# Kernel tuning notes

Hardware: AMD Instinct MI355X
Metric: run time of the kernel (lower is better)

The kernel has to match this reference:

```python
import jax, jax.numpy as jnp
import numpy as np

N_NODES = 20000
N_EDGES = 160000
IN_DIM = 2048
HID = 512


def setup_inputs() -> dict:
    key = jax.random.key(0)
    ks = jax.random.split(key, 12)
    s1 = 1.0 / np.sqrt(IN_DIM)
    s2 = 1.0 / np.sqrt(HID)
    return {
        "x": jax.random.normal(ks[0], (N_NODES, IN_DIM), dtype=jnp.float32),
        "edge_index": jax.random.randint(ks[1], (2, N_EDGES), 0, N_NODES, dtype=jnp.int64),
        "W1": jax.random.uniform(ks[2], (IN_DIM, HID), jnp.float32, -s1, s1),
        "b1": jax.random.uniform(ks[3], (HID,), jnp.float32, -s1, s1),
        "W2": jax.random.uniform(ks[4], (HID, HID), jnp.float32, -s2, s2),
        "b2": jax.random.uniform(ks[5], (HID,), jnp.float32, -s2, s2),
        "Wg": jax.random.uniform(ks[6], (HID, HID), jnp.float32, -s2, s2),
        "bg": jax.random.uniform(ks[7], (HID,), jnp.float32, -s2, s2),
        "Wa": jax.random.uniform(ks[8], (HID, 1), jnp.float32, -s2, s2),
        "ba": jax.random.uniform(ks[9], (1,), jnp.float32, -s2, s2),
    }


def reference(x, edge_index, W1, b1, W2, b2, Wg, bg, Wa, ba):
    # GINConv (eps=0): h = MLP((1+eps)*x + sum_{j in N(i)} x_j)
    src, dst = edge_index[0], edge_index[1]
    agg = jax.ops.segment_sum(x[src], dst, num_segments=x.shape[0])  # [N, IN_DIM]
    h = x + agg
    h = jnp.maximum(h @ W1 + b1, 0.0) @ W2 + b2  # [N, HID]
    # Gated attention pooling scores
    A = jnp.tanh(h @ Wg + bg)                    # [N, HID]
    alpha = (A @ Wa + ba)[:, 0]                  # [N]
    att_scores = jax.nn.softmax(alpha, axis=0)   # softmax over all nodes
    return (h, att_scores)
```

## Files before the change

### kernel.cpp

```cpp
#include <hip/hip_runtime.h>

typedef __attribute__((ext_vector_type(8))) __bf16 bf16x8;
typedef __attribute__((ext_vector_type(4))) float f32x4;
typedef __attribute__((ext_vector_type(8))) unsigned short u16x8;

__device__ __forceinline__ unsigned short f2b(float f) {
    union { float f; unsigned u; } v; v.f = f;
    unsigned r = v.u + 0x7FFFu + ((v.u >> 16) & 1u);
    return (unsigned short)(r >> 16);
}

__device__ __forceinline__ unsigned swz(int row, int s) {
    return (unsigned)((row * 64 + s * 16) ^ ((row & 8) << 2));
}

#define GLDS(g, l) __builtin_amdgcn_global_load_lds(                        \
    (const __attribute__((address_space(1))) void*)(g),                     \
    (__attribute__((address_space(3))) void*)(l), 16, 0, 0)

__global__ __launch_bounds__(256) void convw_pre_kernel(const float* __restrict__ W,
                                                        char* __restrict__ out, int K) {
    int t = blockIdx.x * 256 + threadIdx.x;
    if (t >= K * 512) return;
    int k = t >> 9, n = t & 511;
    int cb = n >> 8, r = n & 255, tt = k >> 5, s = (k & 31) >> 3, e = k & 7;
    size_t off = ((size_t)cb * (K >> 5) + tt) * 16384 + swz(r, s) + e * 2;
    *(unsigned short*)(out + off) = f2b(W[t]);
}

__global__ __launch_bounds__(256) void count_kernel(const int* __restrict__ dst,
                                                    int* __restrict__ counts, int E) {
    int e = blockIdx.x * 256 + threadIdx.x;
    if (e < E) atomicAdd(&counts[dst[e]], 1);
}

__global__ __launch_bounds__(1024) void scan_kernel(const int* __restrict__ counts,
                                                    int* __restrict__ offs, int N) {
    __shared__ int wsum[16], wpre[16];
    const int CH = 20;
    int tid = threadIdx.x, lane = tid & 63, wv = tid >> 6;
    int base = tid * CH;
    int s = 0;
    for (int i = 0; i < CH; i++) { int idx = base + i; s += (idx < N) ? counts[idx] : 0; }
    int run = s;
#pragma unroll
    for (int o = 1; o < 64; o <<= 1) { int v = __shfl_up(run, o, 64); if (lane >= o) run += v; }
    if (lane == 63) wsum[wv] = run;
    __syncthreads();
    if (tid == 0) { int acc = 0; for (int w = 0; w < 16; w++) { wpre[w] = acc; acc += wsum[w]; } }
    __syncthreads();
    int pre = wpre[wv] + (run - s);
    for (int i = 0; i < CH; i++) {
        int idx = base + i;
        if (idx <= N) offs[idx] = pre;
        pre += (idx < N) ? counts[idx] : 0;
    }
}

__global__ __launch_bounds__(256) void bucket_kernel(const int* __restrict__ src,
                                                     const int* __restrict__ dst,
                                                     const int* __restrict__ offs,
                                                     int* __restrict__ cursor,
                                                     int* __restrict__ eids, int E) {
    int e = blockIdx.x * 256 + threadIdx.x;
    if (e >= E) return;
    int d = dst[e];
    int pos = atomicAdd(&cursor[d], 1);
    eids[offs[d] + pos] = src[e];
}

__global__ __launch_bounds__(256) void gather_h1_kernel(const float* __restrict__ y,
                                                        const int* __restrict__ offs,
                                                        const int* __restrict__ eids,
                                                        const float* __restrict__ b1,
                                                        unsigned short* __restrict__ h1b,
                                                        int N) {
    int node = blockIdx.x * 2 + (threadIdx.x >> 7);
    if (node >= N) return;
    int c = (threadIdx.x & 127) << 2;
    float4 s = *(const float4*)(y + (size_t)node * 512 + c);
    int beg = offs[node], end = offs[node + 1];
    for (int k = beg; k < end; k++) {
        int sn = eids[k];
        const float4 v = *(const float4*)(y + (size_t)sn * 512 + c);
        s.x += v.x; s.y += v.y; s.z += v.z; s.w += v.w;
    }
    const float4 b = *(const float4*)(b1 + c);
    ushort4 o;
    o.x = f2b(fmaxf(s.x + b.x, 0.f));
    o.y = f2b(fmaxf(s.y + b.y, 0.f));
    o.z = f2b(fmaxf(s.z + b.z, 0.f));
    o.w = f2b(fmaxf(s.w + b.w, 0.f));
    ((ushort4*)h1b)[((size_t)node * 512 + c) >> 2] = o;
}

template <int KDIM, int AMODE, int EPI>
__global__ __launch_bounds__(256) void gemm_sec(const void* __restrict__ Asrc,
                                                const char* __restrict__ Bpre,
                                                const float* __restrict__ bias,
                                                float* __restrict__ Cf,
                                                char* __restrict__ hbpre,
                                                const float* __restrict__ Wa,
                                                float* __restrict__ alphaOut,
                                                int M) {
    constexpr int NT = KDIM / 32;
    __shared__ char smem[40960];
    const int tid = threadIdx.x, lane = tid & 63, wv = tid >> 6;
    const int fr = lane & 15, sec = lane >> 4, hi4 = (lane >> 4) * 4;
    const long row0 = (long)blockIdx.x * 64;
    const int cb = blockIdx.y;
    const char* Bp = Bpre + (size_t)cb * NT * 16384;

    f32x4 acc[4][4];
#pragma unroll
    for (int m = 0; m < 4; m++)
#pragma unroll
        for (int n = 0; n < 4; n++)
#pragma unroll
            for (int r = 0; r < 4; r++) acc[m][n][r] = 0.f;

    const int as_ = tid & 3, ar_ = tid >> 2;
    const unsigned awz = swz(ar_, as_);
    long arow = row0 + ar_; if (arow > (long)M - 1) arow = M - 1;
    const float* ApF = (const float*)Asrc + arow * KDIM + as_ * 8;
    const char*  ApH = (const char*)Asrc + arow * (KDIM * 2) + as_ * 16;
    const char*  ApT = (const char*)Asrc + (size_t)blockIdx.x * 65536;

#define ASEC(b) (smem + (b) * 4096)
#define BSEC(b) (smem + 8192 + (b) * 16384)
#define STAGE_B(buf, t) do {                                              \
        const char* src_ = Bp + (size_t)(t) * 16384;                      \
        _Pragma("unroll") for (int c_ = 0; c_ < 4; c_++)                  \
            GLDS(src_ + tid * 16 + c_ * 4096, BSEC(buf) + tid * 16 + c_ * 4096); \
    } while (0)

    STAGE_B(0, 0);
    if constexpr (AMODE == 0) {
        float4 a0 = *(const float4*)(ApF), a1 = *(const float4*)(ApF + 4);
        u16x8 o; o[0]=f2b(a0.x); o[1]=f2b(a0.y); o[2]=f2b(a0.z); o[3]=f2b(a0.w);
        o[4]=f2b(a1.x); o[5]=f2b(a1.y); o[6]=f2b(a1.z); o[7]=f2b(a1.w);
        *(u16x8*)(ASEC(0) + awz) = o;
    } else if constexpr (AMODE == 1) {
        u16x8 v = *(const u16x8*)(ApH);
        *(u16x8*)(ASEC(0) + awz) = v;
    } else {
        GLDS(ApT + tid * 16, ASEC(0) + tid * 16);
    }
    __syncthreads();

    for (int t = 0; t < NT; t++) {
        const int cur = t & 1, nxt = cur ^ 1;
        const bool more = (t + 1 < NT);
        float4 a0, a1; u16x8 av;
        if (more) {
            STAGE_B(nxt, t + 1);
            if constexpr (AMODE == 0) {
                a0 = *(const float4*)(ApF + (t + 1) * 32);
                a1 = *(const float4*)(ApF + (t + 1) * 32 + 4);
            } else if constexpr (AMODE == 1) {
                av = *(const u16x8*)(ApH + (t + 1) * 64);
            } else {
                GLDS(ApT + (size_t)(t + 1) * 4096 + tid * 16, ASEC(nxt) + tid * 16);
            }
        }
        bf16x8 wf[4], xf[4];
#pragma unroll
        for (int m = 0; m < 4; m++)
            wf[m] = *(const bf16x8*)(BSEC(cur) + swz(wv * 64 + m * 16 + fr, sec));
#pragma unroll
        for (int n = 0; n < 4; n++)
            xf[n] = *(const bf16x8*)(ASEC(cur) + swz(n * 16 + fr, sec));
#pragma unroll
        for (int m = 0; m < 4; m++)
#pragma unroll
            for (int n = 0; n < 4; n++)
                acc[m][n] = __builtin_amdgcn_mfma_f32_16x16x32_bf16(wf[m], xf[n], acc[m][n], 0, 0, 0);
        if (more) {
            if constexpr (AMODE == 0) {
                u16x8 o; o[0]=f2b(a0.x); o[1]=f2b(a0.y); o[2]=f2b(a0.z); o[3]=f2b(a0.w);
                o[4]=f2b(a1.x); o[5]=f2b(a1.y); o[6]=f2b(a1.z); o[7]=f2b(a1.w);
                *(u16x8*)(ASEC(nxt) + awz) = o;
            } else if constexpr (AMODE == 1) {
                *(u16x8*)(ASEC(nxt) + awz) = av;
            }
        }
        __syncthreads();
    }

    if constexpr (EPI == 0) {
#pragma unroll
        for (int n = 0; n < 4; n++) {
            long node = row0 + n * 16 + fr;
            if (node < M) {
#pragma unroll
                for (int m = 0; m < 4; m++)
                    *(f32x4*)(Cf + node * 512 + cb * 256 + wv * 64 + m * 16 + hi4) = acc[m][n];
            }
        }
    } else if constexpr (EPI == 1) {
#pragma unroll
        for (int n = 0; n < 4; n++) {
            int nodeloc = n * 16 + fr;
            long node = row0 + nodeloc;
#pragma unroll
            for (int m = 0; m < 4; m++) {
                int hc = cb * 256 + wv * 64 + m * 16 + hi4;
                f32x4 bv = *(const f32x4*)(bias + hc);
                f32x4 v = acc[m][n] + bv;
                if (node < M) *(f32x4*)(Cf + node * 512 + hc) = v;
                ushort4 o; o.x = f2b(v[0]); o.y = f2b(v[1]); o.z = f2b(v[2]); o.w = f2b(v[3]);
                int tt = hc >> 5, ss = (hc & 31) >> 3, e = hc & 7;
                *(ushort4*)(hbpre + (size_t)blockIdx.x * 65536 + (size_t)tt * 4096 +
                            swz(nodeloc, ss) + e * 2) = o;
            }
        }
    } else {
        float* aS = (float*)smem;
        if (tid < 64) aS[tid] = 0.f;
        __syncthreads();
#pragma unroll
        for (int n = 0; n < 4; n++) {
            float s = 0.f;
#pragma unroll
            for (int m = 0; m < 4; m++) {
                int gc = cb * 256 + wv * 64 + m * 16 + hi4;
                f32x4 bgv = *(const f32x4*)(bias + gc);
                f32x4 wav = *(const f32x4*)(Wa + gc);
#pragma unroll
                for (int r = 0; r < 4; r++)
                    s += tanhf(acc[m][n][r] + bgv[r]) * wav[r];
            }
            atomicAdd(&aS[n * 16 + fr], s);
        }
        __syncthreads();
        if (tid < 64) {
            long node = row0 + tid;
            if (node < M) atomicAdd(&alphaOut[node], aS[tid]);
        }
    }
#undef ASEC
#undef BSEC
#undef STAGE_B
}

__global__ __launch_bounds__(1024) void softmax_kernel(const float* __restrict__ alpha,
                                                       float* __restrict__ att, int N) {
    __shared__ float red[16];
    __shared__ float bc[2];
    int tid = threadIdx.x, lane = tid & 63, wv = tid >> 6;
    float m = -3.4e38f;
    for (int i = tid; i < N; i += 1024) m = fmaxf(m, alpha[i]);
#pragma unroll
    for (int o = 32; o > 0; o >>= 1) m = fmaxf(m, __shfl_xor(m, o, 64));
    if (lane == 0) red[wv] = m;
    __syncthreads();
    if (tid == 0) {
        float mm = red[0];
        for (int i = 1; i < 16; i++) mm = fmaxf(mm, red[i]);
        bc[0] = mm;
    }
    __syncthreads();
    float Mx = bc[0];
    float s = 0.f;
    for (int i = tid; i < N; i += 1024) s += expf(alpha[i] - Mx);
#pragma unroll
    for (int o = 32; o > 0; o >>= 1) s += __shfl_xor(s, o, 64);
    if (lane == 0) red[wv] = s;
    __syncthreads();
    if (tid == 0) {
        float ss = 0.f;
        for (int i = 0; i < 16; i++) ss += red[i];
        bc[1] = ss;
    }
    __syncthreads();
    float inv = 1.f / bc[1];
    for (int i = tid; i < N; i += 1024) att[i] = expf(alpha[i] - Mx) * inv;
}

extern "C" void kernel_launch(void* const* d_in, const int* in_sizes, int n_in,
                              void* d_out, int out_size, void* d_ws, size_t ws_size,
                              hipStream_t stream) {
    const float* x  = (const float*)d_in[0];
    const int*   ei = (const int*)d_in[1];
    const float* W1 = (const float*)d_in[2];
    const float* b1 = (const float*)d_in[3];
    const float* W2 = (const float*)d_in[4];
    const float* b2 = (const float*)d_in[5];
    const float* Wg = (const float*)d_in[6];
    const float* bg = (const float*)d_in[7];
    const float* Wa = (const float*)d_in[8];

    const int M = 20000, IN = 2048, H = 512, E = 160000;

    char* ws = (char*)d_ws;
    float* y      = (float*)ws;
    char*  W1p    = ws + 40960000;
    char*  W2p    = ws + 43057152;
    char*  Wgp    = ws + 43581440;
    unsigned short* h1b = (unsigned short*)(ws + 44105728);
    char*  hbpre  = ws + 64585728;
    float* alpha  = (float*)(ws + 85098496);
    int*   counts = (int*)(ws + 85178496);
    int*   offs   = (int*)(ws + 85258496);
    int*   cursor = (int*)(ws + 85338504);
    int*   eids   = (int*)(ws + 85418504);

    float* hout = (float*)d_out;
    float* att  = hout + (size_t)M * H;

    convw_pre_kernel<<<4096, 256, 0, stream>>>(W1, W1p, IN);
    convw_pre_kernel<<<1024, 256, 0, stream>>>(W2, W2p, H);
    convw_pre_kernel<<<1024, 256, 0, stream>>>(Wg, Wgp, H);

    hipMemsetAsync(counts, 0, M * 4, stream);
    count_kernel<<<(E + 255) / 256, 256, 0, stream>>>(ei + E, counts, E);
    scan_kernel<<<1, 1024, 0, stream>>>(counts, offs, M);
    hipMemsetAsync(cursor, 0, M * 4, stream);
    bucket_kernel<<<(E + 255) / 256, 256, 0, stream>>>(ei, ei + E, offs, cursor, eids, E);

    gemm_sec<2048, 0, 0><<<dim3(313, 2), 256, 0, stream>>>(x, W1p, nullptr, y, nullptr, nullptr, nullptr, M);

    gather_h1_kernel<<<10000, 256, 0, stream>>>(y, offs, eids, b1, h1b, M);

    gemm_sec<512, 1, 1><<<dim3(313, 2), 256, 0, stream>>>(h1b, W2p, b2, hout, hbpre, nullptr, nullptr, M);

    hipMemsetAsync(alpha, 0, M * 4, stream);
    gemm_sec<512, 2, 2><<<dim3(313, 2), 256, 0, stream>>>(hbpre, Wgp, bg, nullptr, nullptr, Wa, alpha, M);

    softmax_kernel<<<1, 1024, 0, stream>>>(alpha, att, M);
}
```

Measured before the change: 273.2 us.

## Triple-buffer GEMM K-loop with two-stage-ahead prefetch and manual waitcnt

Converts the bf16 MFMA GEMM main loop from double to triple buffering. It prefetches A and B tiles two K-steps ahead and replaces __syncthreads with explicit s_waitcnt vmcnt counts plus s_barrier. The goal is to hide global-load latency better behind the MFMAs. In exchange, LDS per block grows to 60KB, which may cut occupancy, and the hand-counted vmcnt values are fragile if the compiler reorders or merges loads.

```diff
diff --git a/kernel.cpp b/kernel.cpp
--- a/kernel.cpp
+++ b/kernel.cpp
@@ -104,7 +104,7 @@
                                                 float* __restrict__ alphaOut,
                                                 int M) {
     constexpr int NT = KDIM / 32;
-    __shared__ char smem[40960];
+    __shared__ char smem[61440];
     const int tid = threadIdx.x, lane = tid & 63, wv = tid >> 6;
     const int fr = lane & 15, sec = lane >> 4, hi4 = (lane >> 4) * 4;
     const long row0 = (long)blockIdx.x * 64;
@@ -126,65 +126,95 @@
     const char*  ApH = (const char*)Asrc + arow * (KDIM * 2) + as_ * 16;
     const char*  ApT = (const char*)Asrc + (size_t)blockIdx.x * 65536;
 
-#define ASEC(b) (smem + (b) * 4096)
-#define BSEC(b) (smem + 8192 + (b) * 16384)
-#define STAGE_B(buf, t) do {                                              \
+#define ASEC(s) (smem + (s) * 4096)
+#define BSEC(s) (smem + 12288 + (s) * 16384)
+#define STAGE_B(s, t) do {                                                \
         const char* src_ = Bp + (size_t)(t) * 16384;                      \
         _Pragma("unroll") for (int c_ = 0; c_ < 4; c_++)                  \
-            GLDS(src_ + tid * 16 + c_ * 4096, BSEC(buf) + tid * 16 + c_ * 4096); \
+            GLDS(src_ + tid * 16 + c_ * 4096, BSEC(s) + tid * 16 + c_ * 4096); \
     } while (0)
 
-    STAGE_B(0, 0);
+    float4 aP0, aP1, aN0, aN1;
+    u16x8  aPv, aNv;
+
     if constexpr (AMODE == 0) {
-        float4 a0 = *(const float4*)(ApF), a1 = *(const float4*)(ApF + 4);
-        u16x8 o; o[0]=f2b(a0.x); o[1]=f2b(a0.y); o[2]=f2b(a0.z); o[3]=f2b(a0.w);
-        o[4]=f2b(a1.x); o[5]=f2b(a1.y); o[6]=f2b(a1.z); o[7]=f2b(a1.w);
+        aP0 = *(const float4*)(ApF); aP1 = *(const float4*)(ApF + 4);
+        STAGE_B(0, 0);
+        u16x8 o; o[0]=f2b(aP0.x); o[1]=f2b(aP0.y); o[2]=f2b(aP0.z); o[3]=f2b(aP0.w);
+        o[4]=f2b(aP1.x); o[5]=f2b(aP1.y); o[6]=f2b(aP1.z); o[7]=f2b(aP1.w);
         *(u16x8*)(ASEC(0) + awz) = o;
+        aP0 = *(const float4*)(ApF + 32); aP1 = *(const float4*)(ApF + 36);
+        STAGE_B(1, 1);
+        asm volatile("s_waitcnt vmcnt(6) lgkmcnt(0)" ::: "memory");
     } else if constexpr (AMODE == 1) {
-        u16x8 v = *(const u16x8*)(ApH);
-        *(u16x8*)(ASEC(0) + awz) = v;
+        aPv = *(const u16x8*)(ApH);
+        STAGE_B(0, 0);
+        *(u16x8*)(ASEC(0) + awz) = aPv;
+        aPv = *(const u16x8*)(ApH + 64);
+        STAGE_B(1, 1);
+        asm volatile("s_waitcnt vmcnt(5) lgkmcnt(0)" ::: "memory");
     } else {
         GLDS(ApT + tid * 16, ASEC(0) + tid * 16);
-    }
-    __syncthreads();
-
+        STAGE_B(0, 0);
+        GLDS(ApT + 4096 + tid * 16, ASEC(1) + tid * 16);
+        STAGE_B(1, 1);
+        asm volatile("s_waitcnt vmcnt(5) lgkmcnt(0)" ::: "memory");
+    }
+    __builtin_amdgcn_s_barrier();
+    __builtin_amdgcn_sched_barrier(0);
+
+    int sc = 0, s1 = 1, s2 = 2;
     for (int t = 0; t < NT; t++) {
-        const int cur = t & 1, nxt = cur ^ 1;
-        const bool more = (t + 1 < NT);
-        float4 a0, a1; u16x8 av;
-        if (more) {
-            STAGE_B(nxt, t + 1);
+        const bool pf = (t + 2 < NT);
+        if (pf) {
             if constexpr (AMODE == 0) {
-                a0 = *(const float4*)(ApF + (t + 1) * 32);
-                a1 = *(const float4*)(ApF + (t + 1) * 32 + 4);
+                aN0 = *(const float4*)(ApF + (t + 2) * 32);
+                aN1 = *(const float4*)(ApF + (t + 2) * 32 + 4);
             } else if constexpr (AMODE == 1) {
-                av = *(const u16x8*)(ApH + (t + 1) * 64);
+                aNv = *(const u16x8*)(ApH + (size_t)(t + 2) * 64);
             } else {
-                GLDS(ApT + (size_t)(t + 1) * 4096 + tid * 16, ASEC(nxt) + tid * 16);
+                GLDS(ApT + (size_t)(t + 2) * 4096 + tid * 16, ASEC(s2) + tid * 16);
+            }
+            STAGE_B(s2, t + 2);
+        }
+        if constexpr (AMODE == 0) {
+            if (t + 1 < NT) {
+                u16x8 o; o[0]=f2b(aP0.x); o[1]=f2b(aP0.y); o[2]=f2b(aP0.z); o[3]=f2b(aP0.w);
+                o[4]=f2b(aP1.x); o[5]=f2b(aP1.y); o[6]=f2b(aP1.z); o[7]=f2b(aP1.w);
+                *(u16x8*)(ASEC(s1) + awz) = o;
+                aP0 = aN0; aP1 = aN1;
+            }
+        } else if constexpr (AMODE == 1) {
+            if (t + 1 < NT) {
+                *(u16x8*)(ASEC(s1) + awz) = aPv;
+                aPv = aNv;
             }
         }
         bf16x8 wf[4], xf[4];
 #pragma unroll
         for (int m = 0; m < 4; m++)
-            wf[m] = *(const bf16x8*)(BSEC(cur) + swz(wv * 64 + m * 16 + fr, sec));
+            wf[m] = *(const bf16x8*)(BSEC(sc) + swz(wv * 64 + m * 16 + fr, sec));
 #pragma unroll
         for (int n = 0; n < 4; n++)
-            xf[n] = *(const bf16x8*)(ASEC(cur) + swz(n * 16 + fr, sec));
+            xf[n] = *(const bf16x8*)(ASEC(sc) + swz(n * 16 + fr, sec));
 #pragma unroll
         for (int m = 0; m < 4; m++)
 #pragma unroll
             for (int n = 0; n < 4; n++)
                 acc[m][n] = __builtin_amdgcn_mfma_f32_16x16x32_bf16(wf[m], xf[n], acc[m][n], 0, 0, 0);
-        if (more) {
-            if constexpr (AMODE == 0) {
-                u16x8 o; o[0]=f2b(a0.x); o[1]=f2b(a0.y); o[2]=f2b(a0.z); o[3]=f2b(a0.w);
-                o[4]=f2b(a1.x); o[5]=f2b(a1.y); o[6]=f2b(a1.z); o[7]=f2b(a1.w);
-                *(u16x8*)(ASEC(nxt) + awz) = o;
-            } else if constexpr (AMODE == 1) {
-                *(u16x8*)(ASEC(nxt) + awz) = av;
-            }
-        }
-        __syncthreads();
+        if (t + 1 < NT) {
+            if (pf) {
+                if constexpr (AMODE == 0)
+                    asm volatile("s_waitcnt vmcnt(6) lgkmcnt(0)" ::: "memory");
+                else
+                    asm volatile("s_waitcnt vmcnt(5) lgkmcnt(0)" ::: "memory");
+            } else {
+                asm volatile("s_waitcnt vmcnt(0) lgkmcnt(0)" ::: "memory");
+            }
+            __builtin_amdgcn_s_barrier();
+            __builtin_amdgcn_sched_barrier(0);
+        }
+        int tmp = sc; sc = s1; s1 = s2; s2 = tmp;
     }
 
     if constexpr (EPI == 0) {
@@ -215,6 +245,7 @@
             }
         }
     } else {
+        __syncthreads();
         float* aS = (float*)smem;
         if (tid < 64) aS[tid] = 0.f;
         __syncthreads();
```

New measurement: 302.0 us. +10.6%, slower.
